# Performance work log

Measured on AMD Instinct MI355X. Metric: run time of the kernel, lower is better.

The kernel has to match this reference:

```python
import jax, jax.numpy as jnp
import numpy as np

IN_FEATURES = 512
HIDDEN_DIM = 512
B, S = 8, 2048


def setup_inputs() -> dict:
    key = jax.random.key(0)
    ks = jax.random.split(key, 7)
    sc_in = 1.0 / np.sqrt(IN_FEATURES)
    return {
        "x": jax.random.normal(ks[0], (B, S, IN_FEATURES), dtype=jnp.float32),
        "Wq": jax.random.normal(ks[1], (IN_FEATURES, HIDDEN_DIM), dtype=jnp.float32) * sc_in,
        "bq": jax.random.normal(ks[2], (HIDDEN_DIM,), dtype=jnp.float32) * 0.01,
        "Wk": jax.random.normal(ks[3], (IN_FEATURES, HIDDEN_DIM), dtype=jnp.float32) * sc_in,
        "bk": jax.random.normal(ks[4], (HIDDEN_DIM,), dtype=jnp.float32) * 0.01,
        "Wv": jax.random.normal(ks[5], (IN_FEATURES, HIDDEN_DIM), dtype=jnp.float32) * sc_in,
        "bv": jax.random.normal(ks[6], (HIDDEN_DIM,), dtype=jnp.float32) * 0.01,
    }


def reference(x, Wq, bq, Wk, bk, Wv, bv):
    # x: [B, S, in_features]
    q = jnp.einsum("bsf,fh->bsh", x, Wq) + bq  # [B, S, H]
    k = jnp.einsum("bsf,fh->bsh", x, Wk) + bk
    v = jnp.einsum("bsf,fh->bsh", x, Wv) + bv
    scale = 1.0 / jnp.sqrt(jnp.asarray(q.shape[-1], dtype=q.dtype))
    scores = jnp.einsum("bqh,bkh->bqk", q, k) * scale  # [B, S, S]
    weights = jax.nn.softmax(scores, axis=-1)
    return jnp.einsum("bqk,bkh->bqh", weights, v)  # [B, S, H]
```

## Files before the change

kernel.cpp:

```cpp
#include <hip/hip_runtime.h>
#include <hip/hip_bf16.h>

typedef __bf16 bf16;
typedef __bf16 bf16x8 __attribute__((ext_vector_type(8)));
typedef float  f32x4  __attribute__((ext_vector_type(4)));

#define MFMA16(a,b,c) __builtin_amdgcn_mfma_f32_16x16x32_bf16((a),(b),(c),0,0,0)

static const int BATCH = 8;
static const int SEQ   = 2048;
static const int HID   = 512;
static const int MTOT  = BATCH * SEQ;

__device__ __forceinline__ void gl2lds16(const void* g, void* l) {
    __builtin_amdgcn_global_load_lds(
        (const __attribute__((address_space(1))) void*)g,
        (__attribute__((address_space(3))) void*)l, 16, 0, 0);
}

__global__ void k_convert_x(const float* __restrict__ x, bf16* __restrict__ xb, int n4) {
    int i = blockIdx.x * blockDim.x + threadIdx.x;
    int stride = gridDim.x * blockDim.x;
    for (; i < n4; i += stride) {
        float4 v = ((const float4*)x)[i];
        union { bf16 h[4]; uint2 u; } o;
        o.h[0] = (bf16)v.x; o.h[1] = (bf16)v.y; o.h[2] = (bf16)v.z; o.h[3] = (bf16)v.w;
        ((uint2*)xb)[i] = o.u;
    }
}

__global__ void k_transpose_w(const float* __restrict__ Wq, const float* __restrict__ Wk,
                              const float* __restrict__ Wv, bf16* __restrict__ wt) {
    int z = blockIdx.z;
    const float* W = (z == 0) ? Wq : (z == 1) ? Wk : Wv;
    bf16* WT = wt + (size_t)z * HID * HID;
    __shared__ float tile[32][33];
    int t  = threadIdx.x;
    int tx = t & 31, ty = t >> 5;
    int f0 = blockIdx.y * 32, h0 = blockIdx.x * 32;
    for (int i = 0; i < 32; i += 8)
        tile[ty + i][tx] = W[(size_t)(f0 + ty + i) * HID + h0 + tx];
    __syncthreads();
    for (int i = 0; i < 32; i += 8)
        WT[(size_t)(h0 + ty + i) * HID + f0 + tx] = (bf16)tile[tx][ty + i];
}

__global__ __launch_bounds__(256) void
k_qkv(const bf16* __restrict__ xb, const bf16* __restrict__ wt,
      const float* __restrict__ bq, const float* __restrict__ bk, const float* __restrict__ bv,
      bf16* __restrict__ qb, bf16* __restrict__ kb, bf16* __restrict__ vt) {
    __shared__ __align__(16) char sm[65536];
    int z = blockIdx.z;
    const bf16*  WT   = wt + (size_t)z * HID * HID;
    const float* bias = (z == 0) ? bq : (z == 1) ? bk : bv;
    float scale = (z == 0) ? 0.044194173824159216f : 1.0f;

    int m0 = blockIdx.y * 128, n0 = blockIdx.x * 128;
    int t = threadIdx.x;
    int w = t >> 6, lane = t & 63, quad = lane >> 4, l15 = lane & 15;
    int wr = w >> 1, wc = w & 1;

    int rowA = t >> 3;
    int chS  = (t & 7) ^ (rowA & 7);
    const char* xga = (const char*)xb + ((size_t)(m0 + rowA) * 512 + chS * 8) * 2;
    const char* wga = (const char*)WT + ((size_t)(n0 + rowA) * 512 + chS * 8) * 2;

    const char* aK0 = sm + (wr * 64 + l15) * 128 + ((quad ^ (l15 & 7)) * 16);
    const char* aK1 = sm + (wr * 64 + l15) * 128 + (((4 + quad) ^ (l15 & 7)) * 16);
    const char* bK0 = sm + 16384 + (wc * 64 + l15) * 128 + ((quad ^ (l15 & 7)) * 16);
    const char* bK1 = sm + 16384 + (wc * 64 + l15) * 128 + (((4 + quad) ^ (l15 & 7)) * 16);

    f32x4 acc[4][4] = {};

#define QSTAGE(S)                                                             \
    {                                                                         \
        _Pragma("unroll")                                                     \
        for (int i = 0; i < 4; i++)                                           \
            gl2lds16(xga + i * 32768, sm + (S) * 32768 + i * 4096 + w * 1024);\
        _Pragma("unroll")                                                     \
        for (int i = 0; i < 4; i++)                                           \
            gl2lds16(wga + i * 32768,                                         \
                     sm + (S) * 32768 + 16384 + i * 4096 + w * 1024);         \
        xga += 128; wga += 128;                                               \
    }

#define QCOMP(CUR)                                                            \
    {                                                                         \
        bf16x8 af[4], bfr[4];                                                 \
        _Pragma("unroll")                                                     \
        for (int mt = 0; mt < 4; mt++)                                        \
            af[mt] = *(const bf16x8*)(aK0 + mt * 2048 + (CUR) * 32768);       \
        _Pragma("unroll")                                                     \
        for (int nt = 0; nt < 4; nt++)                                        \
            bfr[nt] = *(const bf16x8*)(bK0 + nt * 2048 + (CUR) * 32768);      \
        _Pragma("unroll")                                                     \
        for (int mt = 0; mt < 4; mt++)                                        \
            _Pragma("unroll")                                                 \
            for (int nt = 0; nt < 4; nt++)                                    \
                acc[mt][nt] = MFMA16(af[mt], bfr[nt], acc[mt][nt]);           \
        _Pragma("unroll")                                                     \
        for (int mt = 0; mt < 4; mt++)                                        \
            af[mt] = *(const bf16x8*)(aK1 + mt * 2048 + (CUR) * 32768);       \
        _Pragma("unroll")                                                     \
        for (int nt = 0; nt < 4; nt++)                                        \
            bfr[nt] = *(const bf16x8*)(bK1 + nt * 2048 + (CUR) * 32768);      \
        _Pragma("unroll")                                                     \
        for (int mt = 0; mt < 4; mt++)                                        \
            _Pragma("unroll")                                                 \
            for (int nt = 0; nt < 4; nt++)                                    \
                acc[mt][nt] = MFMA16(af[mt], bfr[nt], acc[mt][nt]);           \
    }

    QSTAGE(0);
    __syncthreads();
    for (int ii = 0; ii < 4; ii++) {
        QSTAGE(1);
        QCOMP(0);
        __syncthreads();
        if (ii < 3) QSTAGE(0);
        QCOMP(1);
        __syncthreads();
    }
#undef QSTAGE
#undef QCOMP

    if (z < 2) {
        bf16* out = (z == 0) ? qb : kb;
#pragma unroll
        for (int nt = 0; nt < 4; nt++) {
            int col = n0 + wc * 64 + nt * 16 + l15;
            float bc = bias[col];
#pragma unroll
            for (int mt = 0; mt < 4; mt++) {
                int rowb = m0 + wr * 64 + mt * 16 + quad * 4;
#pragma unroll
                for (int r = 0; r < 4; r++) {
                    float v = (acc[mt][nt][r] + bc) * scale;
                    out[(size_t)(rowb + r) * HID + col] = (bf16)v;
                }
            }
        }
    } else {
        bf16* st = (bf16*)sm;
#pragma unroll
        for (int nt = 0; nt < 4; nt++) {
            int colL = wc * 64 + nt * 16 + l15;
            float bc = bias[n0 + colL];
#pragma unroll
            for (int mt = 0; mt < 4; mt++) {
                int rowL = wr * 64 + mt * 16 + quad * 4;
#pragma unroll
                for (int r = 0; r < 4; r++)
                    st[(size_t)colL * 136 + rowL + r] = (bf16)(acc[mt][nt][r] + bc);
            }
        }
        __syncthreads();
        int b  = m0 >> 11;
        int s0 = m0 & 2047;
        bf16* vbase = vt + ((size_t)b * HID + n0) * SEQ + s0;
#pragma unroll
        for (int i = 0; i < 8; i++) {
            int p = i * 256 + t;
            int colL = p >> 4, ch = p & 15;
            *(uint4*)((char*)vbase + (size_t)colL * SEQ * 2 + ch * 16) =
                *(const uint4*)&st[(size_t)colL * 136 + ch * 8];
        }
    }
}

__global__ __launch_bounds__(512, 2) void
k_attn(const bf16* __restrict__ qb, const bf16* __restrict__ kbuf,
       const bf16* __restrict__ vt, float* __restrict__ out) {
    __shared__ __align__(16) char smem[136832];
    char* sm = smem;

    int j = blockIdx.x;
    int b = j & 7, qblk = j >> 3;
    int t = threadIdx.x, w = t >> 6, lane = t & 63, quad = lane >> 4, l15 = lane & 15;
    int rg = w & 3, kg = w >> 2;

    const bf16* Qrow   = qb + ((size_t)b * SEQ + qblk * 64 + rg * 16) * HID;
    const bf16* Kbase  = kbuf + (size_t)b * SEQ * HID;
    const bf16* VTbase = vt + (size_t)b * HID * SEQ;

    const char* kE = sm + (kg * 16 + l15) * 1024 + ((quad ^ (l15 & 7)) * 16);
    const char* kO = sm + (kg * 16 + l15) * 1024 + (((4 + quad) ^ (l15 & 7)) * 16);
    char*       pW = sm + 131072 + (rg * 16 + quad * 4) * 80 + (kg * 16 + l15) * 2;
    const char* pR = sm + 131072 + l15 * 80 + quad * 16;
    const char* vA = sm + 65536 + w * 4096 + l15 * 64 + ((quad ^ (l15 & 3)) * 16);
    float*      mlx = (float*)(sm + 136192);

    const char* kgp = (const char*)Kbase + w * 1024 + ((lane ^ w) * 16);
    const char* vgp = (const char*)VTbase + (w * 16 + (lane >> 2)) * 4096
                      + (((lane & 3) ^ ((lane >> 2) & 3)) * 16);

    bf16x8 qf[16];
#pragma unroll
    for (int kt = 0; kt < 16; kt++)
        qf[kt] = *(const bf16x8*)&Qrow[(size_t)l15 * HID + kt * 32 + quad * 8];

    float l_acc[4] = {0.f, 0.f, 0.f, 0.f};
    f32x4 o_acc[16] = {};

    const int NIT = SEQ / 32;

#define STAGE(S)                                                              \
    {                                                                         \
        _Pragma("unroll")                                                     \
        for (int jj = 0; jj < 4; jj++)                                        \
            gl2lds16(kgp + jj * 8192,                                         \
                     sm + (S) * 32768 + jj * 8192 + w * 1024);                \
        _Pragma("unroll")                                                     \
        for (int jj = 0; jj < 4; jj++)                                        \
            gl2lds16(vgp + jj * 524288,                                       \
                     sm + 65536 + (S) * 32768 + jj * 8192 + w * 1024);        \
        kgp += 32768; vgp += 64;                                              \
    }

#define QKP(CUR)                                                              \
    {                                                                         \
        f32x4 sa = {}, sb = {};                                               \
        _Pragma("unroll")                                                     \
        for (int kt = 0; kt < 16; kt += 2) {                                  \
            bf16x8 kfe = *(const bf16x8*)(kE + (kt >> 1) * 128 + (CUR) * 32768); \
            bf16x8 kfo = *(const bf16x8*)(kO + (kt >> 1) * 128 + (CUR) * 32768); \
            sa = MFMA16(qf[kt], kfe, sa);                                     \
            sb = MFMA16(qf[kt + 1], kfo, sb);                                 \
        }                                                                     \
        _Pragma("unroll")                                                     \
        for (int r = 0; r < 4; r++) {                                         \
            float p = __expf(sa[r] + sb[r] - 8.0f);                           \
            l_acc[r] += p;                                                    \
            *(bf16*)(pW + r * 80) = (bf16)p;                                  \
        }                                                                     \
    }

#define PV(CUR)                                                               \
    {                                                                         \
        bf16x8 pa0 = *(const bf16x8*)(pR + 0 * 1280);                         \
        bf16x8 pa1 = *(const bf16x8*)(pR + 1 * 1280);                         \
        bf16x8 pa2 = *(const bf16x8*)(pR + 2 * 1280);                         \
        bf16x8 pa3 = *(const bf16x8*)(pR + 3 * 1280);                         \
        _Pragma("unroll")                                                     \
        for (int hs = 0; hs < 4; hs++) {                                      \
            bf16x8 vf = *(const bf16x8*)(vA + hs * 1024 + (CUR) * 32768);     \
            o_acc[0 * 4 + hs] = MFMA16(pa0, vf, o_acc[0 * 4 + hs]);           \
            o_acc[1 * 4 + hs] = MFMA16(pa1, vf, o_acc[1 * 4 + hs]);           \
            o_acc[2 * 4 + hs] = MFMA16(pa2, vf, o_acc[2 * 4 + hs]);           \
            o_acc[3 * 4 + hs] = MFMA16(pa3, vf, o_acc[3 * 4 + hs]);           \
        }                                                                     \
    }

    STAGE(0);
    __syncthreads();

    for (int ii = 0; ii < NIT / 2; ii++) {
        QKP(0);
        __syncthreads();
        STAGE(1);
        PV(0);
        __syncthreads();

        QKP(1);
        __syncthreads();
        if (ii < NIT / 2 - 1) STAGE(0);
        PV(1);
        __syncthreads();
    }

    float lw[4];
#pragma unroll
    for (int r = 0; r < 4; r++) {
        float v = l_acc[r];
        for (int d = 1; d < 16; d <<= 1) v += __shfl_xor(v, d, 64);
        lw[r] = v;
    }
    if (l15 == 0)
#pragma unroll
        for (int r = 0; r < 4; r++) mlx[kg * 64 + rg * 16 + quad * 4 + r] = lw[r];
    __syncthreads();

    float lt[4][4];
#pragma unroll
    for (int rgp = 0; rgp < 4; rgp++)
#pragma unroll
        for (int r = 0; r < 4; r++) {
            int row = rgp * 16 + quad * 4 + r;
            lt[rgp][r] = 1.0f / (mlx[row] + mlx[64 + row]);
        }
    float* obase = out + ((size_t)b * SEQ + qblk * 64) * HID + w * 64;
#pragma unroll
    for (int rgp = 0; rgp < 4; rgp++)
#pragma unroll
        for (int hs = 0; hs < 4; hs++)
#pragma unroll
            for (int r = 0; r < 4; r++)
                obase[(size_t)(rgp * 16 + quad * 4 + r) * HID + hs * 16 + l15] =
                    o_acc[rgp * 4 + hs][r] * lt[rgp][r];
#undef STAGE
#undef QKP
#undef PV
}

extern "C" void kernel_launch(void* const* d_in, const int* in_sizes, int n_in,
                              void* d_out, int out_size, void* d_ws, size_t ws_size,
                              hipStream_t stream) {
    const float* x  = (const float*)d_in[0];
    const float* Wq = (const float*)d_in[1];
    const float* bq = (const float*)d_in[2];
    const float* Wk = (const float*)d_in[3];
    const float* bk = (const float*)d_in[4];
    const float* Wv = (const float*)d_in[5];
    const float* bv = (const float*)d_in[6];
    float* out = (float*)d_out;

    char* ws = (char*)d_ws;
    const size_t SZ_XB = (size_t)MTOT * HID * 2;
    const size_t SZ_WT = (size_t)HID * HID * 2;
    bf16* xb = (bf16*)(ws);
    bf16* wt = (bf16*)(ws + SZ_XB);
    bf16* qb = (bf16*)(ws + SZ_XB + 3 * SZ_WT);
    bf16* kb = (bf16*)(ws + SZ_XB + 3 * SZ_WT + SZ_XB);
    bf16* vt = (bf16*)(ws + SZ_XB + 3 * SZ_WT + 2 * SZ_XB);

    k_convert_x<<<2048, 256, 0, stream>>>(x, xb, MTOT * HID / 4);
    k_transpose_w<<<dim3(16, 16, 3), 256, 0, stream>>>(Wq, Wk, Wv, wt);
    k_qkv<<<dim3(4, 128, 3), 256, 0, stream>>>(xb, wt, bq, bk, bv, qb, kb, vt);
    k_attn<<<256, 512, 0, stream>>>(qb, kb, vt, out);
}
```

Before: 277.2 us.

## Reschedule attention loop barriers to prefetch next KV tile earlier, add MFMA priority

Reorders the double-buffered attention main loop so the next K/V tile's global-to-LDS load is issued right after the barrier, before the QK^T MFMAs rather than after them. The plain __syncthreads are replaced by hand-built barriers that wait only on vmcnt or lgkmcnt as needed, with sched_barrier fences. s_setprio raises wave priority around the MFMA loops so matrix work is favoured over other waves' memory issue. The aim is more overlap of load latency with compute and less barrier stall, at the risk of buffer-reuse races if the wait counts are wrong.

```diff
diff --git a/kernel.cpp b/kernel.cpp
--- a/kernel.cpp
+++ b/kernel.cpp
@@ -220,6 +220,7 @@
 #define QKP(CUR)                                                              \
     {                                                                         \
         f32x4 sa = {}, sb = {};                                               \
+        __builtin_amdgcn_s_setprio(1);                                        \
         _Pragma("unroll")                                                     \
         for (int kt = 0; kt < 16; kt += 2) {                                  \
             bf16x8 kfe = *(const bf16x8*)(kE + (kt >> 1) * 128 + (CUR) * 32768); \
@@ -227,6 +228,7 @@
             sa = MFMA16(qf[kt], kfe, sa);                                     \
             sb = MFMA16(qf[kt + 1], kfo, sb);                                 \
         }                                                                     \
+        __builtin_amdgcn_s_setprio(0);                                        \
         _Pragma("unroll")                                                     \
         for (int r = 0; r < 4; r++) {                                         \
             float p = __expf(sa[r] + sb[r] - 8.0f);                           \
@@ -241,6 +243,7 @@
         bf16x8 pa1 = *(const bf16x8*)(pR + 1 * 1280);                         \
         bf16x8 pa2 = *(const bf16x8*)(pR + 2 * 1280);                         \
         bf16x8 pa3 = *(const bf16x8*)(pR + 3 * 1280);                         \
+        __builtin_amdgcn_s_setprio(1);                                        \
         _Pragma("unroll")                                                     \
         for (int hs = 0; hs < 4; hs++) {                                      \
             bf16x8 vf = *(const bf16x8*)(vA + hs * 1024 + (CUR) * 32768);     \
@@ -249,23 +252,40 @@
             o_acc[2 * 4 + hs] = MFMA16(pa2, vf, o_acc[2 * 4 + hs]);           \
             o_acc[3 * 4 + hs] = MFMA16(pa3, vf, o_acc[3 * 4 + hs]);           \
         }                                                                     \
+        __builtin_amdgcn_s_setprio(0);                                        \
+    }
+
+#define BAR_A()                                                               \
+    {                                                                         \
+        asm volatile("s_waitcnt vmcnt(0)" ::: "memory");                      \
+        __builtin_amdgcn_sched_barrier(0);                                    \
+        __builtin_amdgcn_s_barrier();                                         \
+        __builtin_amdgcn_sched_barrier(0);                                    \
+    }
+
+#define BAR_B()                                                               \
+    {                                                                         \
+        asm volatile("s_waitcnt lgkmcnt(0)" ::: "memory");                    \
+        __builtin_amdgcn_sched_barrier(0);                                    \
+        __builtin_amdgcn_s_barrier();                                         \
+        __builtin_amdgcn_sched_barrier(0);                                    \
     }
 
     STAGE(0);
-    __syncthreads();
 
     for (int ii = 0; ii < NIT / 2; ii++) {
+        BAR_A();
+        STAGE(1);
+        __builtin_amdgcn_sched_barrier(0);
         QKP(0);
-        __syncthreads();
-        STAGE(1);
+        BAR_B();
         PV(0);
-        __syncthreads();
-
+        BAR_A();
+        if (ii < NIT / 2 - 1) STAGE(0);
+        __builtin_amdgcn_sched_barrier(0);
         QKP(1);
-        __syncthreads();
-        if (ii < NIT / 2 - 1) STAGE(0);
+        BAR_B();
         PV(1);
-        __syncthreads();
     }
 
     float lw[4];
@@ -275,6 +295,7 @@
         for (int d = 1; d < 16; d <<= 1) v += __shfl_xor(v, d, 64);
         lw[r] = v;
     }
+    __syncthreads();
     if (l15 == 0)
 #pragma unroll
         for (int r = 0; r < 4; r++) mlx[kg * 64 + rg * 16 + quad * 4 + r] = lw[r];
@@ -300,6 +321,8 @@
 #undef STAGE
 #undef QKP
 #undef PV
+#undef BAR_A
+#undef BAR_B
 }
 
 extern "C" void kernel_launch(void* const* d_in, const int* in_sizes, int n_in,
```

After: 235.6 us. -15.0%, faster.
